# Optimization experiments

Hardware: AMD Instinct MI355X
Metric: run time of the kernel (lower is better)

Reference implementation:

```python
import jax, jax.numpy as jnp
import numpy as np

N = 100000   # nodes
R = 8        # relations
E = 800000   # edges per relation
D = 128      # in_feat == out_feat
B = 4        # num bases
L = 2        # ngnn layers


def setup_inputs() -> dict:
    key = jax.random.key(0)
    ks = jax.random.split(key, 8)
    x = jax.random.normal(ks[0], (N, D), dtype=jnp.float32)
    edge_src = jax.random.randint(ks[1], (R, E), 0, N, dtype=jnp.int64)
    edge_dst = jax.random.randint(ks[2], (R, E), 0, N, dtype=jnp.int64)
    scale = 1.0 / np.sqrt(D)
    w_comp = jax.random.normal(ks[3], (R, B), dtype=jnp.float32) * 0.3
    bases = jax.random.normal(ks[4], (B, D, D), dtype=jnp.float32) * scale
    loop_weight = jax.random.normal(ks[5], (D, D), dtype=jnp.float32) * scale
    h_bias = jnp.zeros((D,), dtype=jnp.float32)
    ngnn_w = jax.random.normal(ks[6], (L, D, D), dtype=jnp.float32) * scale
    return {"x": x, "edge_src": edge_src, "edge_dst": edge_dst,
            "w_comp": w_comp, "bases": bases, "loop_weight": loop_weight,
            "h_bias": h_bias, "ngnn_w": ngnn_w}


def reference(x, edge_src, edge_dst, w_comp, bases, loop_weight, h_bias, ngnn_w):
    # basis-decomposed per-relation weights: [R, D, D]
    weight = jnp.einsum('rb,bio->rio', w_comp, bases)
    h = jnp.zeros((N, D), dtype=x.dtype)
    # per-relation GraphConv, norm='right' (mean over in-degree, clamp min 1),
    # in_feat == out_feat so DGL aggregates first then applies weight;
    # HeteroGraphConv sums relation outputs for the shared dst type.
    for r in range(R):
        src, dst = edge_src[r], edge_dst[r]
        msg = jax.ops.segment_sum(x[src], dst, num_segments=N)           # [N, D]
        deg = jax.ops.segment_sum(jnp.ones((E,), x.dtype), dst, num_segments=N)
        agg = msg / jnp.maximum(deg, 1.0)[:, None]
        h = h + agg @ weight[r]
    # self loop + bias + activation
    h = jax.nn.relu(h + x @ loop_weight + h_bias)
    # NGNN MLP (dropout is identity in eval)
    for l in range(ngnn_w.shape[0]):
        h = jax.nn.relu(h @ ngnn_w[l])
    return h
```

## Files before the change

kernel.cpp:

```cpp
#include <hip/hip_runtime.h>
#include <hip/hip_bf16.h>

#define N_NODES 100000
#define R_REL   8
#define E_EDGES 800000
#define D_FEAT  128
#define B_BASES 4
#define RN      (R_REL * N_NODES)
#define RE      (R_REL * E_EDGES)

#define NBKT    784
#define BKT_CAP 9216
#define P1_TPB  256
#define P1_EPT  32
#define P1_CHUNK (P1_TPB * P1_EPT)
#define P1_NWG  ((RE + P1_CHUNK - 1) / P1_CHUNK)

typedef __attribute__((ext_vector_type(8))) short short8;
typedef __attribute__((ext_vector_type(4))) float floatx4;

__global__ __launch_bounds__(1024) void init_cursor_kernel(int* __restrict__ gcursor) {
    int t = threadIdx.x;
    if (t < NBKT) gcursor[t] = t * BKT_CAP;
}

__global__ __launch_bounds__(256) void xcvt_kernel(
    const float* __restrict__ x, uint* __restrict__ xb) {
    int i = blockIdx.x * 256 + threadIdx.x;
    if (i >= N_NODES * 64) return;
    float2 v = *(const float2*)(x + 2 * (size_t)i);
    __hip_bfloat162 h = __float22bfloat162_rn(v);
    xb[i] = *(uint*)&h;
}

__global__ __launch_bounds__(256) void wcvt_kernel(
    const float* __restrict__ bases, const float* __restrict__ loopw,
    unsigned short* __restrict__ wT) {
    int idx = blockIdx.x * 256 + threadIdx.x;
    if (idx >= 128 * 640) return;
    int n = idx / 640, k = idx % 640;
    float v = (k < 512) ? bases[(size_t)k * 128 + n] : loopw[(size_t)(k - 512) * 128 + n];
    __hip_bfloat16 h = __float2bfloat16(v);
    wT[idx] = *(unsigned short*)&h;
}

__global__ __launch_bounds__(256) void wcvt2_kernel(
    const float* __restrict__ ngnn_w, unsigned short* __restrict__ wT2) {
    int idx = blockIdx.x * 256 + threadIdx.x;
    if (idx >= 2 * 128 * 128) return;
    int l = idx >> 14, rem = idx & 16383;
    int n = rem >> 7, k = rem & 127;
    float v = ngnn_w[(size_t)l * 16384 + (size_t)k * 128 + n];
    __hip_bfloat16 h = __float2bfloat16(v);
    wT2[idx] = *(unsigned short*)&h;
}

__global__ __launch_bounds__(256) void p1_kernel(
    const int* __restrict__ src, const int* __restrict__ dst,
    int* __restrict__ gcursor, int* __restrict__ ebuf2) {
    __shared__ int hist[NBKT];
    __shared__ int cnt2[NBKT];
    __shared__ int basebkt[NBKT];
    __shared__ int lofs[NBKT];
    __shared__ int aux[256];
    __shared__ int recs[P1_CHUNK];
    __shared__ unsigned short bb[P1_CHUNK];
    int t = threadIdx.x;
    for (int i = t; i < NBKT; i += 256) { hist[i] = 0; cnt2[i] = 0; }
    __syncthreads();

    int e0 = blockIdx.x * P1_CHUNK;
    int rec[P1_EPT];
    int bkt[P1_EPT];
#pragma unroll
    for (int i = 0; i < P1_EPT; ++i) {
        int e = e0 + i * P1_TPB + t;
        if (e < RE) {
            int d = dst[e];
            int s = src[e];
            int r = e / E_EDGES;
            bkt[i] = d >> 7;
            rec[i] = s | ((d & 127) << 17) | (r << 24);
            atomicAdd(&hist[bkt[i]], 1);
        } else bkt[i] = -1;
    }
    __syncthreads();

    int k0 = t * 4;
    int c0 = (k0 + 0 < NBKT) ? hist[k0 + 0] : 0;
    int c1 = (k0 + 1 < NBKT) ? hist[k0 + 1] : 0;
    int c2 = (k0 + 2 < NBKT) ? hist[k0 + 2] : 0;
    int c3 = (k0 + 3 < NBKT) ? hist[k0 + 3] : 0;
    int s1 = c0 + c1, s2 = s1 + c2, s3 = s2 + c3;
    aux[t] = s3;
    __syncthreads();
    int vv = s3;
    for (int off = 1; off < 256; off <<= 1) {
        int yv = (t >= off) ? aux[t - off] : 0;
        __syncthreads();
        vv += yv;
        aux[t] = vv;
        __syncthreads();
    }
    int total = aux[255];
    int texcl = vv - s3;
    if (k0 + 0 < NBKT) lofs[k0 + 0] = texcl;
    if (k0 + 1 < NBKT) lofs[k0 + 1] = texcl + c0;
    if (k0 + 2 < NBKT) lofs[k0 + 2] = texcl + s1;
    if (k0 + 3 < NBKT) lofs[k0 + 3] = texcl + s2;
    __syncthreads();
    for (int i = t; i < NBKT; i += 256) {
        int hv = hist[i];
        basebkt[i] = (hv > 0) ? atomicAdd(&gcursor[i], hv) : 0;
    }
    __syncthreads();

#pragma unroll
    for (int i = 0; i < P1_EPT; ++i) {
        if (bkt[i] >= 0) {
            int p = lofs[bkt[i]] + atomicAdd(&cnt2[bkt[i]], 1);
            recs[p] = rec[i];
            bb[p] = (unsigned short)bkt[i];
        }
    }
    __syncthreads();

    for (int i = t; i < total; i += 256) {
        int b = bb[i];
        int p2 = basebkt[b] + (i - lofs[b]);
        if (p2 < (b + 1) * BKT_CAP) ebuf2[p2] = recs[i];
    }
}

template <bool XB>
__global__ __launch_bounds__(1024, 8) void agg2_kernel(
    const float* __restrict__ x,
    const uint*  __restrict__ xb,
    const int*   __restrict__ gcursor,
    const int*   __restrict__ ebuf2,
    const float* __restrict__ w_comp,
    __hip_bfloat162* __restrict__ y) {
    __shared__ int raw[BKT_CAP];
    __shared__ int sorted[BKT_CAP];
    __shared__ int cursors[1024];
    __shared__ int segbeg[1024];
    const int t = threadIdx.x;
    const int bucket = blockIdx.x;

    int cnt = gcursor[bucket] - bucket * BKT_CAP;
    if (cnt > BKT_CAP) cnt = BKT_CAP;
    const int* brec = ebuf2 + (size_t)bucket * BKT_CAP;
    for (int i = t; i < cnt; i += 1024) raw[i] = brec[i];
    cursors[t] = 0;
    __syncthreads();

    for (int i = t; i < cnt; i += 1024) {
        int rec = raw[i];
        int key = ((rec >> 17) & 127) * 8 + ((rec >> 24) & 7);
        atomicAdd(&cursors[key], 1);
    }
    __syncthreads();

    int deg = cursors[t];
    int* aux = sorted;
    aux[t] = deg;
    __syncthreads();
    int vv = deg;
    for (int off = 1; off < 1024; off <<= 1) {
        int yv = (t >= off) ? aux[t - off] : 0;
        __syncthreads();
        vv += yv;
        aux[t] = vv;
        __syncthreads();
    }
    int beg = vv - deg;
    cursors[t] = beg;
    segbeg[t]  = beg;
    __syncthreads();

    for (int i = t; i < cnt; i += 1024) {
        int rec = raw[i];
        int key = ((rec >> 17) & 127) * 8 + ((rec >> 24) & 7);
        int pos = atomicAdd(&cursors[key], 1);
        sorted[pos] = rec & 0x1FFFF;
    }
    __syncthreads();

    const int wid = t >> 6, lane = t & 63;
    const float* xp  = x + 2 * lane;
    const uint*  xbp = xb + lane;
    for (int nn = 0; nn < 8; ++nn) {
        int nl = wid * 8 + nn;
        int node = bucket * 128 + nl;
        int key0 = nl * 8;
        float2 acc[B_BASES];
#pragma unroll
        for (int b = 0; b < B_BASES; ++b) acc[b] = make_float2(0.f, 0.f);
#pragma unroll
        for (int r = 0; r < R_REL; ++r) {
            int b0 = segbeg[key0 + r];
            int e0 = cursors[key0 + r];
            int d = e0 - b0;
            float inv = 1.0f / (float)(d > 1 ? d : 1);
            float ax = 0.f, ay = 0.f;
            int i = b0;
            for (; i + 3 < e0; i += 4) {
                int s0 = sorted[i], s1 = sorted[i + 1], s2 = sorted[i + 2], s3 = sorted[i + 3];
                if (XB) {
                    uint u0 = xbp[(size_t)s0 * 64];
                    uint u1 = xbp[(size_t)s1 * 64];
                    uint u2 = xbp[(size_t)s2 * 64];
                    uint u3 = xbp[(size_t)s3 * 64];
                    ax += (__uint_as_float(u0 << 16) + __uint_as_float(u1 << 16))
                        + (__uint_as_float(u2 << 16) + __uint_as_float(u3 << 16));
                    ay += (__uint_as_float(u0 & 0xFFFF0000u) + __uint_as_float(u1 & 0xFFFF0000u))
                        + (__uint_as_float(u2 & 0xFFFF0000u) + __uint_as_float(u3 & 0xFFFF0000u));
                } else {
                    float2 a = *(const float2*)(xp + (size_t)s0 * D_FEAT);
                    float2 b = *(const float2*)(xp + (size_t)s1 * D_FEAT);
                    float2 cc = *(const float2*)(xp + (size_t)s2 * D_FEAT);
                    float2 d2 = *(const float2*)(xp + (size_t)s3 * D_FEAT);
                    ax += (a.x + b.x) + (cc.x + d2.x);
                    ay += (a.y + b.y) + (cc.y + d2.y);
                }
            }
            for (; i < e0; ++i) {
                int s = sorted[i];
                if (XB) {
                    uint u = xbp[(size_t)s * 64];
                    ax += __uint_as_float(u << 16);
                    ay += __uint_as_float(u & 0xFFFF0000u);
                } else {
                    float2 a = *(const float2*)(xp + (size_t)s * D_FEAT);
                    ax += a.x; ay += a.y;
                }
            }
#pragma unroll
            for (int b = 0; b < B_BASES; ++b) {
                float coef = w_comp[r * B_BASES + b] * inv;
                acc[b].x = fmaf(coef, ax, acc[b].x);
                acc[b].y = fmaf(coef, ay, acc[b].y);
            }
        }
        if (node < N_NODES) {
#pragma unroll
            for (int b = 0; b < B_BASES; ++b)
                y[(size_t)node * 256 + b * 64 + lane] = __float22bfloat162_rn(acc[b]);
        }
    }
}

__global__ __launch_bounds__(256) void gemm_big_mfma(
    const short* __restrict__ y,
    const float* __restrict__ x,
    const unsigned short* __restrict__ wT,
    const float* __restrict__ bias,
    unsigned short* __restrict__ hb1) {
    const int wave = threadIdx.x >> 6;
    const int lane = threadIdx.x & 63;
    const int quad = lane >> 4;
    const int l16  = lane & 15;
    const int row0 = blockIdx.x * 64 + wave * 16;
    int arow = row0 + l16;
    if (arow >= N_NODES) arow = N_NODES - 1;

    floatx4 acc[8];
#pragma unroll
    for (int nt = 0; nt < 8; ++nt) acc[nt] = (floatx4){0.f, 0.f, 0.f, 0.f};

    const short* yrow = y + (size_t)arow * 512;
    const float* xrow = x + (size_t)arow * 128;
    const int koff = quad * 8;

    for (int ks = 0; ks < 16; ++ks) {
        int k0 = ks * 32 + koff;
        short8 a = *(const short8*)(yrow + k0);
#pragma unroll
        for (int nt = 0; nt < 8; ++nt) {
            int n = nt * 16 + l16;
            short8 b = *(const short8*)((const short*)wT + (size_t)n * 640 + k0);
            acc[nt] = __builtin_amdgcn_mfma_f32_16x16x32_bf16(a, b, acc[nt], 0, 0, 0);
        }
    }
#pragma unroll
    for (int ks = 0; ks < 4; ++ks) {
        int k0 = ks * 32 + koff;
        float4 fa = *(const float4*)(xrow + k0);
        float4 fb = *(const float4*)(xrow + k0 + 4);
        union { short8 s; uint u[4]; } ua;
        __hip_bfloat162 h0 = __float22bfloat162_rn(make_float2(fa.x, fa.y));
        __hip_bfloat162 h1 = __float22bfloat162_rn(make_float2(fa.z, fa.w));
        __hip_bfloat162 h2 = __float22bfloat162_rn(make_float2(fb.x, fb.y));
        __hip_bfloat162 h3 = __float22bfloat162_rn(make_float2(fb.z, fb.w));
        ua.u[0] = *(uint*)&h0; ua.u[1] = *(uint*)&h1;
        ua.u[2] = *(uint*)&h2; ua.u[3] = *(uint*)&h3;
#pragma unroll
        for (int nt = 0; nt < 8; ++nt) {
            int n = nt * 16 + l16;
            short8 b = *(const short8*)((const short*)wT + (size_t)n * 640 + 512 + k0);
            acc[nt] = __builtin_amdgcn_mfma_f32_16x16x32_bf16(ua.s, b, acc[nt], 0, 0, 0);
        }
    }

#pragma unroll
    for (int nt = 0; nt < 8; ++nt) {
        int n = nt * 16 + l16;
        float bs = bias[n];
#pragma unroll
        for (int i = 0; i < 4; ++i) {
            int m = row0 + quad * 4 + i;
            if (m < N_NODES) {
                float v = fmaxf(acc[nt][i] + bs, 0.f);
                __hip_bfloat16 h = __float2bfloat16(v);
                hb1[(size_t)m * D_FEAT + n] = *(unsigned short*)&h;
            }
        }
    }
}

template <bool OUT_BF16>
__global__ __launch_bounds__(256) void ngnn_mfma(
    const short* __restrict__ A,
    const unsigned short* __restrict__ wTl,
    void* __restrict__ C) {
    const int wave = threadIdx.x >> 6;
    const int lane = threadIdx.x & 63;
    const int quad = lane >> 4;
    const int l16  = lane & 15;
    const int row0 = blockIdx.x * 64 + wave * 16;
    int arow = row0 + l16;
    if (arow >= N_NODES) arow = N_NODES - 1;

    floatx4 acc[8];
#pragma unroll
    for (int nt = 0; nt < 8; ++nt) acc[nt] = (floatx4){0.f, 0.f, 0.f, 0.f};

    const short* ar = A + (size_t)arow * 128;
    const int koff = quad * 8;
#pragma unroll
    for (int ks = 0; ks < 4; ++ks) {
        int k0 = ks * 32 + koff;
        short8 a = *(const short8*)(ar + k0);
#pragma unroll
        for (int nt = 0; nt < 8; ++nt) {
            int n = nt * 16 + l16;
            short8 b = *(const short8*)((const short*)wTl + (size_t)n * 128 + k0);
            acc[nt] = __builtin_amdgcn_mfma_f32_16x16x32_bf16(a, b, acc[nt], 0, 0, 0);
        }
    }

#pragma unroll
    for (int nt = 0; nt < 8; ++nt) {
        int n = nt * 16 + l16;
#pragma unroll
        for (int i = 0; i < 4; ++i) {
            int m = row0 + quad * 4 + i;
            if (m < N_NODES) {
                float v = fmaxf(acc[nt][i], 0.f);
                if (OUT_BF16) {
                    __hip_bfloat16 h = __float2bfloat16(v);
                    ((unsigned short*)C)[(size_t)m * D_FEAT + n] = *(unsigned short*)&h;
                } else {
                    ((float*)C)[(size_t)m * D_FEAT + n] = v;
                }
            }
        }
    }
}

extern "C" void kernel_launch(void* const* d_in, const int* in_sizes, int n_in,
                              void* d_out, int out_size, void* d_ws, size_t ws_size,
                              hipStream_t stream) {
    const float* x           = (const float*)d_in[0];
    const int*   edge_src    = (const int*)d_in[1];
    const int*   edge_dst    = (const int*)d_in[2];
    const float* w_comp      = (const float*)d_in[3];
    const float* bases       = (const float*)d_in[4];
    const float* loop_weight = (const float*)d_in[5];
    const float* h_bias      = (const float*)d_in[6];
    const float* ngnn_w      = (const float*)d_in[7];
    float* out = (float*)d_out;

    char* ws = (char*)d_ws;
    size_t off = 0;
    __hip_bfloat162* y = (__hip_bfloat162*)(ws + off);
    off += (size_t)N_NODES * 512 * 2;
    int* ebuf2 = (int*)(ws + off);
    unsigned short* hb1 = (unsigned short*)(ws + off);
    off += (size_t)NBKT * BKT_CAP * 4;
    int* gcursor = (int*)(ws + off);
    off += 4096;
    unsigned short* wT = (unsigned short*)(ws + off);
    off += (size_t)128 * 640 * 2;
    unsigned short* wT2 = (unsigned short*)(ws + off);
    off += (size_t)2 * 128 * 128 * 2;
    uint* xb = (uint*)(ws + off);
    size_t xb_bytes = (size_t)N_NODES * 64 * 4;
    const bool use_bf16_x = (ws_size >= off + xb_bytes);
    unsigned short* hb2 = use_bf16_x ? (unsigned short*)xb : (unsigned short*)y;

    const int GEMM_GRID = (N_NODES + 63) / 64;

    wcvt_kernel<<<(128 * 640 + 255) / 256, 256, 0, stream>>>(bases, loop_weight, wT);
    wcvt2_kernel<<<(2 * 128 * 128 + 255) / 256, 256, 0, stream>>>(ngnn_w, wT2);
    if (use_bf16_x)
        xcvt_kernel<<<(N_NODES * 64 + 255) / 256, 256, 0, stream>>>(x, xb);

    init_cursor_kernel<<<1, 1024, 0, stream>>>(gcursor);
    p1_kernel<<<P1_NWG, P1_TPB, 0, stream>>>(edge_src, edge_dst, gcursor, ebuf2);

    if (use_bf16_x)
        agg2_kernel<true><<<NBKT, 1024, 0, stream>>>(x, xb, gcursor, ebuf2, w_comp, y);
    else
        agg2_kernel<false><<<NBKT, 1024, 0, stream>>>(x, nullptr, gcursor, ebuf2, w_comp, y);

    gemm_big_mfma<<<GEMM_GRID, 256, 0, stream>>>(
        (const short*)y, x, wT, h_bias, hb1);

    ngnn_mfma<true><<<GEMM_GRID, 256, 0, stream>>>(
        (const short*)hb1, wT2, (void*)hb2);
    ngnn_mfma<false><<<GEMM_GRID, 256, 0, stream>>>(
        (const short*)hb2, wT2 + 128 * 128, (void*)out);
}
```

Before: 704.3 us.

## Slim edge-bucketing kernel registers/LDS and reuse bf16 x in fused GEMM

The edge-bucketing kernel stops holding per-edge records and bucket ids in registers and no longer keeps a per-record bucket array in shared memory. It re-reads src/dst in a second pass and recovers each record's bucket by binary search over the local offsets. Edges per thread drop from 32 to 16, which doubles the workgroup count and cuts LDS and register use so more workgroups can be resident. The self-loop GEMM now reads the precomputed bf16 copy of x instead of converting fp32 on the fly, at the cost of reading edges twice and doing a log-time search per record.

```diff
diff --git a/kernel.cpp b/kernel.cpp
--- a/kernel.cpp
+++ b/kernel.cpp
@@ -12,7 +12,7 @@
 #define NBKT    784
 #define BKT_CAP 9216
 #define P1_TPB  256
-#define P1_EPT  32
+#define P1_EPT  16
 #define P1_CHUNK (P1_TPB * P1_EPT)
 #define P1_NWG  ((RE + P1_CHUNK - 1) / P1_CHUNK)
 
@@ -60,29 +60,18 @@
     int* __restrict__ gcursor, int* __restrict__ ebuf2) {
     __shared__ int hist[NBKT];
     __shared__ int cnt2[NBKT];
-    __shared__ int basebkt[NBKT];
     __shared__ int lofs[NBKT];
     __shared__ int aux[256];
     __shared__ int recs[P1_CHUNK];
-    __shared__ unsigned short bb[P1_CHUNK];
     int t = threadIdx.x;
     for (int i = t; i < NBKT; i += 256) { hist[i] = 0; cnt2[i] = 0; }
     __syncthreads();
 
     int e0 = blockIdx.x * P1_CHUNK;
-    int rec[P1_EPT];
-    int bkt[P1_EPT];
 #pragma unroll
     for (int i = 0; i < P1_EPT; ++i) {
         int e = e0 + i * P1_TPB + t;
-        if (e < RE) {
-            int d = dst[e];
-            int s = src[e];
-            int r = e / E_EDGES;
-            bkt[i] = d >> 7;
-            rec[i] = s | ((d & 127) << 17) | (r << 24);
-            atomicAdd(&hist[bkt[i]], 1);
-        } else bkt[i] = -1;
+        if (e < RE) atomicAdd(&hist[dst[e] >> 7], 1);
     }
     __syncthreads();
 
@@ -111,24 +100,32 @@
     __syncthreads();
     for (int i = t; i < NBKT; i += 256) {
         int hv = hist[i];
-        basebkt[i] = (hv > 0) ? atomicAdd(&gcursor[i], hv) : 0;
+        hist[i] = (hv > 0) ? atomicAdd(&gcursor[i], hv) : 0;
     }
     __syncthreads();
 
 #pragma unroll
     for (int i = 0; i < P1_EPT; ++i) {
-        if (bkt[i] >= 0) {
-            int p = lofs[bkt[i]] + atomicAdd(&cnt2[bkt[i]], 1);
-            recs[p] = rec[i];
-            bb[p] = (unsigned short)bkt[i];
+        int e = e0 + i * P1_TPB + t;
+        if (e < RE) {
+            int d = dst[e];
+            int s = src[e];
+            int r = e / E_EDGES;
+            int b = d >> 7;
+            int pos = lofs[b] + atomicAdd(&cnt2[b], 1);
+            recs[pos] = s | ((d & 127) << 17) | (r << 24);
         }
     }
     __syncthreads();
 
     for (int i = t; i < total; i += 256) {
-        int b = bb[i];
-        int p2 = basebkt[b] + (i - lofs[b]);
-        if (p2 < (b + 1) * BKT_CAP) ebuf2[p2] = recs[i];
+        int lo = 0, hi = NBKT;
+        while (hi - lo > 1) {
+            int mid = (lo + hi) >> 1;
+            if (lofs[mid] <= i) lo = mid; else hi = mid;
+        }
+        int p = hist[lo] + (i - lofs[lo]);
+        if (p < (lo + 1) * BKT_CAP) ebuf2[p] = recs[i];
     }
 }
 
@@ -250,9 +247,11 @@
     }
 }
 
+template <bool XB>
 __global__ __launch_bounds__(256) void gemm_big_mfma(
     const short* __restrict__ y,
     const float* __restrict__ x,
+    const short* __restrict__ xbs,
     const unsigned short* __restrict__ wT,
     const float* __restrict__ bias,
     unsigned short* __restrict__ hb1) {
@@ -269,7 +268,6 @@
     for (int nt = 0; nt < 8; ++nt) acc[nt] = (floatx4){0.f, 0.f, 0.f, 0.f};
 
     const short* yrow = y + (size_t)arow * 512;
-    const float* xrow = x + (size_t)arow * 128;
     const int koff = quad * 8;
 
     for (int ks = 0; ks < 16; ++ks) {
@@ -285,20 +283,27 @@
 #pragma unroll
     for (int ks = 0; ks < 4; ++ks) {
         int k0 = ks * 32 + koff;
-        float4 fa = *(const float4*)(xrow + k0);
-        float4 fb = *(const float4*)(xrow + k0 + 4);
-        union { short8 s; uint u[4]; } ua;
-        __hip_bfloat162 h0 = __float22bfloat162_rn(make_float2(fa.x, fa.y));
-        __hip_bfloat162 h1 = __float22bfloat162_rn(make_float2(fa.z, fa.w));
-        __hip_bfloat162 h2 = __float22bfloat162_rn(make_float2(fb.x, fb.y));
-        __hip_bfloat162 h3 = __float22bfloat162_rn(make_float2(fb.z, fb.w));
-        ua.u[0] = *(uint*)&h0; ua.u[1] = *(uint*)&h1;
-        ua.u[2] = *(uint*)&h2; ua.u[3] = *(uint*)&h3;
+        short8 a2;
+        if (XB) {
+            a2 = *(const short8*)(xbs + (size_t)arow * 128 + k0);
+        } else {
+            const float* xrow = x + (size_t)arow * 128;
+            float4 fa = *(const float4*)(xrow + k0);
+            float4 fb = *(const float4*)(xrow + k0 + 4);
+            union { short8 s; uint u[4]; } ua;
+            __hip_bfloat162 h0 = __float22bfloat162_rn(make_float2(fa.x, fa.y));
+            __hip_bfloat162 h1 = __float22bfloat162_rn(make_float2(fa.z, fa.w));
+            __hip_bfloat162 h2 = __float22bfloat162_rn(make_float2(fb.x, fb.y));
+            __hip_bfloat162 h3 = __float22bfloat162_rn(make_float2(fb.z, fb.w));
+            ua.u[0] = *(uint*)&h0; ua.u[1] = *(uint*)&h1;
+            ua.u[2] = *(uint*)&h2; ua.u[3] = *(uint*)&h3;
+            a2 = ua.s;
+        }
 #pragma unroll
         for (int nt = 0; nt < 8; ++nt) {
             int n = nt * 16 + l16;
             short8 b = *(const short8*)((const short*)wT + (size_t)n * 640 + 512 + k0);
-            acc[nt] = __builtin_amdgcn_mfma_f32_16x16x32_bf16(ua.s, b, acc[nt], 0, 0, 0);
+            acc[nt] = __builtin_amdgcn_mfma_f32_16x16x32_bf16(a2, b, acc[nt], 0, 0, 0);
         }
     }
 
@@ -414,8 +419,12 @@
     else
         agg2_kernel<false><<<NBKT, 1024, 0, stream>>>(x, nullptr, gcursor, ebuf2, w_comp, y);
 
-    gemm_big_mfma<<<GEMM_GRID, 256, 0, stream>>>(
-        (const short*)y, x, wT, h_bias, hb1);
+    if (use_bf16_x)
+        gemm_big_mfma<true><<<GEMM_GRID, 256, 0, stream>>>(
+            (const short*)y, x, (const short*)xb, wT, h_bias, hb1);
+    else
+        gemm_big_mfma<false><<<GEMM_GRID, 256, 0, stream>>>(
+            (const short*)y, x, nullptr, wT, h_bias, hb1);
 
     ngnn_mfma<true><<<GEMM_GRID, 256, 0, stream>>>(
         (const short*)hb1, wT2, (void*)hb2);
```

After: 727.4 us. 3.3% more time.
